# Performance work log

Hardware: AMD Instinct MI355X
Metric: run time of the kernel (lower is better)

## Reference

```python
import jax, jax.numpy as jnp
import numpy as np

T, B, IN = 216, 16384, 8
H1, H2 = 16, 64


def _lstm_scan(xs, h0, c0, Wih, Whh, bih, bhh):
    # xs: [T, B, D_in]; returns all hidden states [T, B, H]
    def step(carry, x_t):
        h, c = carry
        g = x_t @ Wih.T + bih + h @ Whh.T + bhh  # [B, 4H]
        i, f, gg, o = jnp.split(g, 4, axis=-1)
        c = jax.nn.sigmoid(f) * c + jax.nn.sigmoid(i) * jnp.tanh(gg)
        h = jax.nn.sigmoid(o) * jnp.tanh(c)
        return (h, c), h
    (_, _), hs = jax.lax.scan(step, (h0, c0), xs)
    return hs


def setup_inputs() -> dict:
    key = jax.random.key(0)
    ks = jax.random.split(key, 24)
    def rn(k, shape, std):
        return jax.random.normal(k, shape, dtype=jnp.float32) * std
    # PyTorch LSTMCell/Linear default init: U(-1/sqrt(H), 1/sqrt(H)) -> use uniform
    def un(k, shape, bound):
        return jax.random.uniform(k, shape, dtype=jnp.float32, minval=-bound, maxval=bound)
    b1 = 1.0 / np.sqrt(H1)
    b2 = 1.0 / np.sqrt(H2)
    inp = {
        'x': jax.random.normal(ks[0], (T, B, IN), dtype=jnp.float32),
        # initial states: kaiming_normal_ with fan_in = last dim -> std = sqrt(2/fan_in)
        'h0f': rn(ks[1], (B, H1), np.sqrt(2.0 / H1)),
        'c0f': rn(ks[2], (B, H1), np.sqrt(2.0 / H1)),
        'h0b': rn(ks[3], (B, H1), np.sqrt(2.0 / H1)),
        'c0b': rn(ks[4], (B, H1), np.sqrt(2.0 / H1)),
        'h0m': rn(ks[5], (B, H2), np.sqrt(2.0 / H2)),
        'c0m': rn(ks[6], (B, H2), np.sqrt(2.0 / H2)),
        'Wih_f': un(ks[7], (4 * H1, IN), b1), 'Whh_f': un(ks[8], (4 * H1, H1), b1),
        'bih_f': un(ks[9], (4 * H1,), b1), 'bhh_f': un(ks[10], (4 * H1,), b1),
        'Wih_b': un(ks[11], (4 * H1, IN), b1), 'Whh_b': un(ks[12], (4 * H1, H1), b1),
        'bih_b': un(ks[13], (4 * H1,), b1), 'bhh_b': un(ks[14], (4 * H1,), b1),
        'Wih_m': un(ks[15], (4 * H2, 2 * H1), b2), 'Whh_m': un(ks[16], (4 * H2, H2), b2),
        'bih_m': un(ks[17], (4 * H2,), b2), 'bhh_m': un(ks[18], (4 * H2,), b2),
        'Wd': un(ks[19], (1, H2), b2), 'bd': un(ks[20], (1,), b2),
    }
    return inp


def reference(x, h0f, c0f, h0b, c0b, h0m, c0m,
              Wih_f, Whh_f, bih_f, bhh_f,
              Wih_b, Whh_b, bih_b, bhh_b,
              Wih_m, Whh_m, bih_m, bhh_m,
              Wd, bd):
    # forward direction LSTM over time
    hs_f = _lstm_scan(x, h0f, c0f, Wih_f, Whh_f, bih_f, bhh_f)          # [T,B,16]
    # backward direction: run on reversed sequence, then reverse outputs
    hs_b = _lstm_scan(x[::-1], h0b, c0b, Wih_b, Whh_b, bih_b, bhh_b)[::-1]  # [T,B,16]
    mid_in = jnp.concatenate([hs_f, hs_b], axis=-1)                     # [T,B,32]
    hs_m = _lstm_scan(mid_in, h0m, c0m, Wih_m, Whh_m, bih_m, bhh_m)     # [T,B,64]
    # dropout is identity in inference reference; dense 64->1 per step
    out = jnp.einsum('tbh,oh->tbo', hs_m, Wd) + bd                      # [T,B,1]
    return out[:, :, 0].T                                                # [B,T]
```

## Files before the change

### kernel.cpp

```cpp
#include <hip/hip_runtime.h>

#define TT 216
#define BB 16384
#define LOG2E 1.44269504088896340736f

typedef _Float16 h16;
typedef _Float16 half8 __attribute__((ext_vector_type(8)));
typedef _Float16 h4 __attribute__((ext_vector_type(4)));
typedef float f32x4 __attribute__((ext_vector_type(4)));
typedef int i2 __attribute__((ext_vector_type(2)));
typedef int i4 __attribute__((ext_vector_type(4)));

__device__ __forceinline__ float rcp_f(float v) { return __builtin_amdgcn_rcpf(v); }
__device__ __forceinline__ float ex2(float v)   { return __builtin_amdgcn_exp2f(v); }

__device__ __forceinline__ float lstm_up(float pi, float pf, float pg, float po, float& cs)
{
    float ei = ex2(pi), ef = ex2(pf), eg = ex2(pg), eo = ex2(po);
    float Ei = 1.f + ei, Ef = 1.f + ef, Eg = 1.f + eg, Eo = 1.f + eo;
    float EiEg = Ei * Eg;
    float G = fmaf(2.f * LOG2E, Eg, -4.f * LOG2E);
    float N = fmaf(cs, EiEg, Ef * G);
    cs = N * rcp_f(Ef * EiEg);
    float pc = fminf(cs, 60.f);
    float Ec = 1.f + ex2(pc);
    return (Ec - 2.f) * rcp_f(Eo * Ec);
}

__global__ void prep_kernel(
    const float* __restrict__ Wih_f, const float* __restrict__ Whh_f,
    const float* __restrict__ bih_f, const float* __restrict__ bhh_f,
    const float* __restrict__ Wih_b, const float* __restrict__ Whh_b,
    const float* __restrict__ bih_b, const float* __restrict__ bhh_b,
    const float* __restrict__ Wih_m, const float* __restrict__ Whh_m,
    const float* __restrict__ bih_m, const float* __restrict__ bhh_m,
    h16* __restrict__ W1f, h16* __restrict__ W1b, h16* __restrict__ W2)
{
    int gtid = blockIdx.x * blockDim.x + threadIdx.x;
    int gs = gridDim.x * blockDim.x;
    for (int idx = gtid; idx < 64 * 32; idx += gs) {
        int n = idx >> 5, k = idx & 31;
        float a = ((n >> 4) == 2) ? 2.f * LOG2E : -LOG2E;
        float vf = 0.f, vb = 0.f;
        if (k < 8)        { vf = Wih_f[n * 8 + k];       vb = Wih_b[n * 8 + k]; }
        else if (k < 24)  { vf = Whh_f[n * 16 + k - 8];  vb = Whh_b[n * 16 + k - 8]; }
        else if (k == 24) { vf = bih_f[n] + bhh_f[n];    vb = bih_b[n] + bhh_b[n]; }
        W1f[idx] = (h16)(vf * a);
        W1b[idx] = (h16)(vb * a);
    }
    for (int idx = gtid; idx < 256 * 128; idx += gs) {
        int n = idx >> 7, k = idx & 127;
        float a = ((n >> 6) == 2) ? 2.f * LOG2E : -LOG2E;
        float v = 0.f;
        if (k < 32)       v = Wih_m[n * 32 + k];
        else if (k < 96)  v = Whh_m[n * 64 + k - 32];
        else if (k == 96) v = bih_m[n] + bhh_m[n];
        W2[idx] = (h16)(v * a);
    }
}

__global__ __launch_bounds__(256, 2) void small_lstm_kernel(
    const float* __restrict__ x,
    const float* __restrict__ h0f, const float* __restrict__ c0f,
    const float* __restrict__ h0b, const float* __restrict__ c0b,
    const h16* __restrict__ W1f, const h16* __restrict__ W1b,
    h16* __restrict__ hsf, h16* __restrict__ hsb)
{
    const int tid = threadIdx.x;
    const int wv = tid >> 6, lane = tid & 63;
    const int b = lane & 15, q = lane >> 4;

    const int wgid = blockIdx.x * 4 + wv;
    const int dir  = wgid & 1;
    const int base = (wgid >> 1) * 16;

    const float* h0 = dir ? h0b : h0f;
    const float* c0 = dir ? c0b : c0f;
    const h16* W1   = dir ? W1b : W1f;
    h16* hs = dir ? hsb : hsf;

    half8 wf0 = *(const half8*)(W1 + (0 * 16 + b) * 32 + q * 8);
    half8 wf1 = *(const half8*)(W1 + (1 * 16 + b) * 32 + q * 8);
    half8 wf2 = *(const half8*)(W1 + (2 * 16 + b) * 32 + q * 8);
    half8 wf3 = *(const half8*)(W1 + (3 * 16 + b) * 32 + q * 8);

    f32x4 cv = *(const f32x4*)(c0 + (size_t)(base + b) * 16 + q * 4);
    float cs0 = cv[0] * (2.f * LOG2E);
    float cs1 = cv[1] * (2.f * LOG2E);
    float cs2 = cv[2] * (2.f * LOG2E);
    float cs3 = cv[3] * (2.f * LOG2E);

    const int t0 = dir ? (TT - 1) : 0;

    half8 sf;
    if (q == 0) {
        const float* xp = x + ((size_t)t0 * BB + base + b) * 8;
        f32x4 u0 = *(const f32x4*)xp, u1 = *(const f32x4*)(xp + 4);
        sf[0] = (h16)u0[0]; sf[1] = (h16)u0[1]; sf[2] = (h16)u0[2]; sf[3] = (h16)u0[3];
        sf[4] = (h16)u1[0]; sf[5] = (h16)u1[1]; sf[6] = (h16)u1[2]; sf[7] = (h16)u1[3];
    } else if (q == 3) {
        sf[0] = (h16)1.f;
        sf[1] = (h16)0.f; sf[2] = (h16)0.f; sf[3] = (h16)0.f;
        sf[4] = (h16)0.f; sf[5] = (h16)0.f; sf[6] = (h16)0.f; sf[7] = (h16)0.f;
    } else {
        const float* hp = h0 + (size_t)(base + b) * 16 + (q - 1) * 8;
        f32x4 u0 = *(const f32x4*)hp, u1 = *(const f32x4*)(hp + 4);
        sf[0] = (h16)u0[0]; sf[1] = (h16)u0[1]; sf[2] = (h16)u0[2]; sf[3] = (h16)u0[3];
        sf[4] = (h16)u1[0]; sf[5] = (h16)u1[1]; sf[6] = (h16)u1[2]; sf[7] = (h16)u1[3];
    }

    f32x4 xr[4][2];
    if (q == 0) {
#pragma unroll
        for (int u = 1; u <= 3; ++u) {
            int tl = dir ? (TT - 1 - u) : u;
            const float* xp = x + ((size_t)tl * BB + base + b) * 8;
            xr[u][0] = *(const f32x4*)xp;
            xr[u][1] = *(const f32x4*)(xp + 4);
        }
    }

    for (int it = 0; it < TT / 4; ++it) {
#pragma unroll
        for (int j = 0; j < 4; ++j) {
            const int s = it * 4 + j;
            const int t = dir ? (TT - 1 - s) : s;

            f32x4 z0 = {0.f, 0.f, 0.f, 0.f}, z1 = z0, z2 = z0, z3 = z0;
            z0 = __builtin_amdgcn_mfma_f32_16x16x32_f16(wf0, sf, z0, 0, 0, 0);
            z1 = __builtin_amdgcn_mfma_f32_16x16x32_f16(wf1, sf, z1, 0, 0, 0);
            z2 = __builtin_amdgcn_mfma_f32_16x16x32_f16(wf2, sf, z2, 0, 0, 0);
            z3 = __builtin_amdgcn_mfma_f32_16x16x32_f16(wf3, sf, z3, 0, 0, 0);

            half8 xh;
            {
                const f32x4 u0 = xr[(j + 1) & 3][0], u1 = xr[(j + 1) & 3][1];
                xh[0] = (h16)u0[0]; xh[1] = (h16)u0[1]; xh[2] = (h16)u0[2]; xh[3] = (h16)u0[3];
                xh[4] = (h16)u1[0]; xh[5] = (h16)u1[1]; xh[6] = (h16)u1[2]; xh[7] = (h16)u1[3];
            }
            if (q == 0) {
                int ut = (s + 4 < TT) ? (s + 4) : (TT - 1);
                int tl = dir ? (TT - 1 - ut) : ut;
                const float* xp = x + ((size_t)tl * BB + base + b) * 8;
                xr[j][0] = *(const f32x4*)xp;
                xr[j][1] = *(const f32x4*)(xp + 4);
            }

            float hh0 = lstm_up(z0[0], z1[0], z2[0], z3[0], cs0);
            float hh1 = lstm_up(z0[1], z1[1], z2[1], z3[1], cs1);
            float hh2 = lstm_up(z0[2], z1[2], z2[2], z3[2], cs2);
            float hh3 = lstm_up(z0[3], z1[3], z2[3], z3[3], cs3);

            h4 hv;
            hv[0] = (h16)hh0; hv[1] = (h16)hh1; hv[2] = (h16)hh2; hv[3] = (h16)hh3;
            *(h4*)(hs + ((size_t)t * BB + base + b) * 16 + q * 4) = hv;

            i2 pk = __builtin_bit_cast(i2, hv);
            int sp0 = __builtin_amdgcn_ds_swizzle(pk[0], 0x401F);
            int sp1 = __builtin_amdgcn_ds_swizzle(pk[1], 0x401F);

            i4 nw;
            nw[0] = (q == 1) ? sp0 : pk[0];
            nw[1] = (q == 1) ? sp1 : pk[1];
            nw[2] = (q == 1) ? pk[0] : sp0;
            nw[3] = (q == 1) ? pk[1] : sp1;
            half8 nf = __builtin_bit_cast(half8, nw);

            if (q == 0)      sf = xh;
            else if (q != 3) sf = nf;
        }
    }
}

__global__ __launch_bounds__(256, 4) void mid_lstm_kernel(
    const h16* __restrict__ hsf, const h16* __restrict__ hsb,
    const float* __restrict__ h0m, const float* __restrict__ c0m,
    const h16* __restrict__ W2,
    const float* __restrict__ Wd, const float* __restrict__ bdp,
    float* __restrict__ out)
{
    __shared__ __attribute__((aligned(16))) h16 Xs[2][16][104];
    __shared__ float outbuf[16][55];

    const int tid = threadIdx.x;
    const int base = blockIdx.x * 16;
    const int wv = tid >> 6, lane = tid & 63, col = lane & 15, q = lane >> 4;

    half8 bfr[4][3];
    float bp[4];
#pragma unroll
    for (int p = 0; p < 4; ++p) {
        int n = p * 64 + wv * 16 + col;
#pragma unroll
        for (int kt = 0; kt < 3; ++kt)
            bfr[p][kt] = *(const half8*)(W2 + (size_t)n * 128 + kt * 32 + q * 8);
        bp[p] = (float)W2[(size_t)n * 128 + 96];
    }
    half8 dfr[2];
#pragma unroll
    for (int kt = 0; kt < 2; ++kt)
#pragma unroll
        for (int j = 0; j < 8; ++j)
            dfr[kt][j] = (col == 0) ? (h16)Wd[kt * 32 + q * 8 + j] : (h16)0.f;
    const float bdv = bdp[0];

    float cs[4];
#pragma unroll
    for (int r = 0; r < 4; ++r)
        cs[r] = c0m[(size_t)(base + q * 4 + r) * 64 + wv * 16 + col] * (2.f * LOG2E);

    const h16* hsrc = (wv == 1) ? hsb : hsf;
    const int srow = lane >> 1, su8 = (lane & 1) * 8;
    if (wv < 2 && lane < 32) {
        uint4 v = *(const uint4*)(hsrc + ((size_t)0 * BB + base + srow) * 16 + su8);
        *(uint4*)&Xs[0][srow][wv * 16 + su8] = v;
    }
    {
        int row = tid >> 4, u4 = (tid & 15) * 4;
        float4 v = *(const float4*)(h0m + (size_t)(base + row) * 64 + u4);
        h16* d = &Xs[0][row][32 + u4];
        d[0] = (h16)v.x; d[1] = (h16)v.y; d[2] = (h16)v.z; d[3] = (h16)v.w;
    }
    uint4 ra, rb;
    if (wv < 2 && lane < 32) {
        ra = *(const uint4*)(hsrc + ((size_t)1 * BB + base + srow) * 16 + su8);
        rb = *(const uint4*)(hsrc + ((size_t)2 * BB + base + srow) * 16 + su8);
    }
    __syncthreads();

    for (int t = 0; t < TT; ++t) {
        const int cur = t & 1, nxt = cur ^ 1;
        if (wv < 2 && lane < 32) {
            if (t < TT - 1)
                *(uint4*)&Xs[nxt][srow][wv * 16 + su8] = ra;
            ra = rb;
            int tl = (t + 3 < TT) ? (t + 3) : (TT - 1);
            rb = *(const uint4*)(hsrc + ((size_t)tl * BB + base + srow) * 16 + su8);
        }
        half8 af[3];
#pragma unroll
        for (int kt = 0; kt < 3; ++kt)
            af[kt] = *(const half8*)&Xs[cur][col][kt * 32 + q * 8];
        if (wv == 3 && t > 0) {
            f32x4 z = {0.f, 0.f, 0.f, 0.f};
            z = __builtin_amdgcn_mfma_f32_16x16x32_f16(af[1], dfr[0], z, 0, 0, 0);
            z = __builtin_amdgcn_mfma_f32_16x16x32_f16(af[2], dfr[1], z, 0, 0, 0);
            if (col == 0) {
                int tc = (t - 1) % 54;
#pragma unroll
                for (int r = 0; r < 4; ++r)
                    outbuf[q * 4 + r][tc] = z[r] + bdv;
            }
        }
        f32x4 acc[4];
#pragma unroll
        for (int p = 0; p < 4; ++p) {
            f32x4 z = {bp[p], bp[p], bp[p], bp[p]};
            z = __builtin_amdgcn_mfma_f32_16x16x32_f16(af[0], bfr[p][0], z, 0, 0, 0);
            z = __builtin_amdgcn_mfma_f32_16x16x32_f16(af[1], bfr[p][1], z, 0, 0, 0);
            z = __builtin_amdgcn_mfma_f32_16x16x32_f16(af[2], bfr[p][2], z, 0, 0, 0);
            acc[p] = z;
        }
#pragma unroll
        for (int r = 0; r < 4; ++r) {
            float h = lstm_up(acc[0][r], acc[1][r], acc[2][r], acc[3][r], cs[r]);
            Xs[nxt][q * 4 + r][32 + wv * 16 + col] = (h16)h;
        }
        if (t > 0 && (t % 54) == 0) {
            __syncthreads();
            int off = t - 54;
            for (int idx = tid; idx < 16 * 54; idx += 256) {
                int row = idx / 54, cc = idx - row * 54;
                out[(size_t)(base + row) * TT + off + cc] = outbuf[row][cc];
            }
        }
        __syncthreads();
    }
    if (wv == 3) {
        half8 a1 = *(const half8*)&Xs[0][col][32 + q * 8];
        half8 a2 = *(const half8*)&Xs[0][col][64 + q * 8];
        f32x4 z = {0.f, 0.f, 0.f, 0.f};
        z = __builtin_amdgcn_mfma_f32_16x16x32_f16(a1, dfr[0], z, 0, 0, 0);
        z = __builtin_amdgcn_mfma_f32_16x16x32_f16(a2, dfr[1], z, 0, 0, 0);
        if (col == 0)
#pragma unroll
            for (int r = 0; r < 4; ++r)
                outbuf[q * 4 + r][53] = z[r] + bdv;
    }
    __syncthreads();
    for (int idx = tid; idx < 16 * 54; idx += 256) {
        int row = idx / 54, cc = idx - row * 54;
        out[(size_t)(base + row) * TT + 162 + cc] = outbuf[row][cc];
    }
}

extern "C" void kernel_launch(void* const* d_in, const int* in_sizes, int n_in,
                              void* d_out, int out_size, void* d_ws, size_t ws_size,
                              hipStream_t stream)
{
    const float* x     = (const float*)d_in[0];
    const float* h0f   = (const float*)d_in[1];
    const float* c0f   = (const float*)d_in[2];
    const float* h0b   = (const float*)d_in[3];
    const float* c0b   = (const float*)d_in[4];
    const float* h0m   = (const float*)d_in[5];
    const float* c0m   = (const float*)d_in[6];
    const float* Wih_f = (const float*)d_in[7];
    const float* Whh_f = (const float*)d_in[8];
    const float* bih_f = (const float*)d_in[9];
    const float* bhh_f = (const float*)d_in[10];
    const float* Wih_b = (const float*)d_in[11];
    const float* Whh_b = (const float*)d_in[12];
    const float* bih_b = (const float*)d_in[13];
    const float* bhh_b = (const float*)d_in[14];
    const float* Wih_m = (const float*)d_in[15];
    const float* Whh_m = (const float*)d_in[16];
    const float* bih_m = (const float*)d_in[17];
    const float* bhh_m = (const float*)d_in[18];
    const float* Wd    = (const float*)d_in[19];
    const float* bd    = (const float*)d_in[20];

    char* ws = (char*)d_ws;
    h16* W1f = (h16*)(ws + 0);
    h16* W1b = (h16*)(ws + 4096);
    h16* W2  = (h16*)(ws + 8192);
    h16* hsf = (h16*)(ws + 73728);
    h16* hsb = (h16*)(ws + 73728 + (size_t)TT * BB * 16 * 2);

    prep_kernel<<<64, 256, 0, stream>>>(Wih_f, Whh_f, bih_f, bhh_f,
                                        Wih_b, Whh_b, bih_b, bhh_b,
                                        Wih_m, Whh_m, bih_m, bhh_m,
                                        W1f, W1b, W2);
    small_lstm_kernel<<<512, 256, 0, stream>>>(x, h0f, c0f, h0b, c0b,
                                               W1f, W1b, hsf, hsb);
    mid_lstm_kernel<<<1024, 256, 0, stream>>>(hsf, hsb, h0m, c0m, W2,
                                              Wd, bd, (float*)d_out);
}
```

Baseline: 609.1 us.

## Give each wave its own 16-row batch tile in mid LSTM, registers only

```diff
diff --git a/kernel.cpp b/kernel.cpp
--- a/kernel.cpp
+++ b/kernel.cpp
@@ -34,7 +34,8 @@
     const float* __restrict__ bih_b, const float* __restrict__ bhh_b,
     const float* __restrict__ Wih_m, const float* __restrict__ Whh_m,
     const float* __restrict__ bih_m, const float* __restrict__ bhh_m,
-    h16* __restrict__ W1f, h16* __restrict__ W1b, h16* __restrict__ W2)
+    h16* __restrict__ W1f, h16* __restrict__ W1b,
+    h16* __restrict__ W2p, float* __restrict__ bzp)
 {
     int gtid = blockIdx.x * blockDim.x + threadIdx.x;
     int gs = gridDim.x * blockDim.x;
@@ -48,14 +49,23 @@
         W1f[idx] = (h16)(vf * a);
         W1b[idx] = (h16)(vb * a);
     }
-    for (int idx = gtid; idx < 256 * 128; idx += gs) {
-        int n = idx >> 7, k = idx & 127;
-        float a = ((n >> 6) == 2) ? 2.f * LOG2E : -LOG2E;
-        float v = 0.f;
-        if (k < 32)       v = Wih_m[n * 32 + k];
-        else if (k < 96)  v = Whh_m[n * 64 + k - 32];
-        else if (k == 96) v = bih_m[n] + bhh_m[n];
-        W2[idx] = (h16)(v * a);
+    for (int idx = gtid; idx < 256 * 96; idx += gs) {
+        int pm = idx / 96, k = idx - pm * 96;
+        int p = pm >> 4, m = pm & 15;
+        int g = p >> 2, c = p & 3, qq = m >> 2, r = m & 3;
+        int u = ((c >= 2) ? 32 : 0) + (c & 1) * 4 + 8 * qq + r;
+        int n = g * 64 + u;
+        float a = (g == 2) ? 2.f * LOG2E : -LOG2E;
+        float v = (k < 32) ? Wih_m[n * 32 + k] : Whh_m[n * 64 + (k - 32)];
+        W2p[idx] = (h16)(v * a);
+    }
+    for (int pm = gtid; pm < 256; pm += gs) {
+        int p = pm >> 4, m = pm & 15;
+        int g = p >> 2, c = p & 3, qq = m >> 2, r = m & 3;
+        int u = ((c >= 2) ? 32 : 0) + (c & 1) * 4 + 8 * qq + r;
+        int n = g * 64 + u;
+        float a = (g == 2) ? 2.f * LOG2E : -LOG2E;
+        bzp[pm] = (bih_m[n] + bhh_m[n]) * a;
     }
 }
 
@@ -172,125 +182,125 @@
     }
 }
 
-__global__ __launch_bounds__(256, 4) void mid_lstm_kernel(
+__global__ __launch_bounds__(256, 1) void mid_lstm_kernel(
     const h16* __restrict__ hsf, const h16* __restrict__ hsb,
     const float* __restrict__ h0m, const float* __restrict__ c0m,
-    const h16* __restrict__ W2,
+    const h16* __restrict__ W2p, const float* __restrict__ bzp,
     const float* __restrict__ Wd, const float* __restrict__ bdp,
     float* __restrict__ out)
 {
-    __shared__ __attribute__((aligned(16))) h16 Xs[2][16][104];
-    __shared__ float outbuf[16][55];
-
     const int tid = threadIdx.x;
-    const int base = blockIdx.x * 16;
-    const int wv = tid >> 6, lane = tid & 63, col = lane & 15, q = lane >> 4;
-
-    half8 bfr[4][3];
-    float bp[4];
-#pragma unroll
-    for (int p = 0; p < 4; ++p) {
-        int n = p * 64 + wv * 16 + col;
+    const int wv = tid >> 6, lane = tid & 63;
+    const int b = lane & 15, q = lane >> 4;
+
+    const int wgid = blockIdx.x * 4 + wv;
+    const int base = wgid * 16;
+
+    half8 wfr[16][3];
+#pragma unroll
+    for (int p = 0; p < 16; ++p)
 #pragma unroll
         for (int kt = 0; kt < 3; ++kt)
-            bfr[p][kt] = *(const half8*)(W2 + (size_t)n * 128 + kt * 32 + q * 8);
-        bp[p] = (float)W2[(size_t)n * 128 + 96];
-    }
-    half8 dfr[2];
-#pragma unroll
-    for (int kt = 0; kt < 2; ++kt)
-#pragma unroll
-        for (int j = 0; j < 8; ++j)
-            dfr[kt][j] = (col == 0) ? (h16)Wd[kt * 32 + q * 8 + j] : (h16)0.f;
+            wfr[p][kt] = *(const half8*)(W2p + (size_t)(p * 16 + b) * 96 + kt * 32 + q * 8);
+    f32x4 bz[16];
+#pragma unroll
+    for (int p = 0; p < 16; ++p)
+        bz[p] = *(const f32x4*)(bzp + p * 16 + q * 4);
+    half8 df1, df2;
+#pragma unroll
+    for (int j = 0; j < 8; ++j) {
+        df1[j] = (b == 0) ? (h16)Wd[q * 8 + j] : (h16)0.f;
+        df2[j] = (b == 0) ? (h16)Wd[32 + q * 8 + j] : (h16)0.f;
+    }
     const float bdv = bdp[0];
 
-    float cs[4];
-#pragma unroll
-    for (int r = 0; r < 4; ++r)
-        cs[r] = c0m[(size_t)(base + q * 4 + r) * 64 + wv * 16 + col] * (2.f * LOG2E);
-
-    const h16* hsrc = (wv == 1) ? hsb : hsf;
-    const int srow = lane >> 1, su8 = (lane & 1) * 8;
-    if (wv < 2 && lane < 32) {
-        uint4 v = *(const uint4*)(hsrc + ((size_t)0 * BB + base + srow) * 16 + su8);
-        *(uint4*)&Xs[0][srow][wv * 16 + su8] = v;
-    }
+    f32x4 cs[4];
+#pragma unroll
+    for (int c = 0; c < 4; ++c) {
+        int off = ((c >= 2) ? 32 : 0) + (c & 1) * 4 + 8 * q;
+        f32x4 v = *(const f32x4*)(c0m + (size_t)(base + b) * 64 + off);
+        cs[c][0] = v[0] * (2.f * LOG2E); cs[c][1] = v[1] * (2.f * LOG2E);
+        cs[c][2] = v[2] * (2.f * LOG2E); cs[c][3] = v[3] * (2.f * LOG2E);
+    }
+
+    half8 nf1, nf2;
     {
-        int row = tid >> 4, u4 = (tid & 15) * 4;
-        float4 v = *(const float4*)(h0m + (size_t)(base + row) * 64 + u4);
-        h16* d = &Xs[0][row][32 + u4];
-        d[0] = (h16)v.x; d[1] = (h16)v.y; d[2] = (h16)v.z; d[3] = (h16)v.w;
-    }
-    uint4 ra, rb;
-    if (wv < 2 && lane < 32) {
-        ra = *(const uint4*)(hsrc + ((size_t)1 * BB + base + srow) * 16 + su8);
-        rb = *(const uint4*)(hsrc + ((size_t)2 * BB + base + srow) * 16 + su8);
-    }
-    __syncthreads();
-
-    for (int t = 0; t < TT; ++t) {
-        const int cur = t & 1, nxt = cur ^ 1;
-        if (wv < 2 && lane < 32) {
-            if (t < TT - 1)
-                *(uint4*)&Xs[nxt][srow][wv * 16 + su8] = ra;
-            ra = rb;
-            int tl = (t + 3 < TT) ? (t + 3) : (TT - 1);
-            rb = *(const uint4*)(hsrc + ((size_t)tl * BB + base + srow) * 16 + su8);
+        const float* hp = h0m + (size_t)(base + b) * 64 + q * 8;
+        f32x4 a0 = *(const f32x4*)hp, a1 = *(const f32x4*)(hp + 4);
+        f32x4 a2 = *(const f32x4*)(hp + 32), a3 = *(const f32x4*)(hp + 36);
+        nf1[0] = (h16)a0[0]; nf1[1] = (h16)a0[1]; nf1[2] = (h16)a0[2]; nf1[3] = (h16)a0[3];
+        nf1[4] = (h16)a1[0]; nf1[5] = (h16)a1[1]; nf1[6] = (h16)a1[2]; nf1[7] = (h16)a1[3];
+        nf2[0] = (h16)a2[0]; nf2[1] = (h16)a2[1]; nf2[2] = (h16)a2[2]; nf2[3] = (h16)a2[3];
+        nf2[4] = (h16)a3[0]; nf2[5] = (h16)a3[1]; nf2[6] = (h16)a3[2]; nf2[7] = (h16)a3[3];
+    }
+
+    const h16* hsq = (q < 2) ? hsf : hsb;
+    const size_t hoff = (size_t)(base + b) * 16 + (q & 1) * 8;
+    uint4 hx[4];
+#pragma unroll
+    for (int u = 0; u < 4; ++u)
+        hx[u] = *(const uint4*)(hsq + (size_t)u * BB * 16 + hoff);
+
+    f32x4 ot;
+    for (int it = 0; it < TT / 4; ++it) {
+#pragma unroll
+        for (int j = 0; j < 4; ++j) {
+            const int s = it * 4 + j;
+            const half8 sf0 = __builtin_bit_cast(half8, hx[j]);
+
+            h4 pkc[4];
+#pragma unroll
+            for (int c = 0; c < 4; ++c) {
+                f32x4 z0 = bz[0 * 4 + c], z1 = bz[1 * 4 + c];
+                f32x4 z2 = bz[2 * 4 + c], z3 = bz[3 * 4 + c];
+                z0 = __builtin_amdgcn_mfma_f32_16x16x32_f16(wfr[0 * 4 + c][0], sf0, z0, 0, 0, 0);
+                z0 = __builtin_amdgcn_mfma_f32_16x16x32_f16(wfr[0 * 4 + c][1], nf1, z0, 0, 0, 0);
+                z0 = __builtin_amdgcn_mfma_f32_16x16x32_f16(wfr[0 * 4 + c][2], nf2, z0, 0, 0, 0);
+                z1 = __builtin_amdgcn_mfma_f32_16x16x32_f16(wfr[1 * 4 + c][0], sf0, z1, 0, 0, 0);
+                z1 = __builtin_amdgcn_mfma_f32_16x16x32_f16(wfr[1 * 4 + c][1], nf1, z1, 0, 0, 0);
+                z1 = __builtin_amdgcn_mfma_f32_16x16x32_f16(wfr[1 * 4 + c][2], nf2, z1, 0, 0, 0);
+                z2 = __builtin_amdgcn_mfma_f32_16x16x32_f16(wfr[2 * 4 + c][0], sf0, z2, 0, 0, 0);
+                z2 = __builtin_amdgcn_mfma_f32_16x16x32_f16(wfr[2 * 4 + c][1], nf1, z2, 0, 0, 0);
+                z2 = __builtin_amdgcn_mfma_f32_16x16x32_f16(wfr[2 * 4 + c][2], nf2, z2, 0, 0, 0);
+                z3 = __builtin_amdgcn_mfma_f32_16x16x32_f16(wfr[3 * 4 + c][0], sf0, z3, 0, 0, 0);
+                z3 = __builtin_amdgcn_mfma_f32_16x16x32_f16(wfr[3 * 4 + c][1], nf1, z3, 0, 0, 0);
+                z3 = __builtin_amdgcn_mfma_f32_16x16x32_f16(wfr[3 * 4 + c][2], nf2, z3, 0, 0, 0);
+
+                float c0v = cs[c][0];
+                float hh0 = lstm_up(z0[0], z1[0], z2[0], z3[0], c0v); cs[c][0] = c0v;
+                float c1v = cs[c][1];
+                float hh1 = lstm_up(z0[1], z1[1], z2[1], z3[1], c1v); cs[c][1] = c1v;
+                float c2v = cs[c][2];
+                float hh2 = lstm_up(z0[2], z1[2], z2[2], z3[2], c2v); cs[c][2] = c2v;
+                float c3v = cs[c][3];
+                float hh3 = lstm_up(z0[3], z1[3], z2[3], z3[3], c3v); cs[c][3] = c3v;
+
+                h4 pk;
+                pk[0] = (h16)hh0; pk[1] = (h16)hh1; pk[2] = (h16)hh2; pk[3] = (h16)hh3;
+                pkc[c] = pk;
+            }
+            {
+                i2 p0 = __builtin_bit_cast(i2, pkc[0]), p1 = __builtin_bit_cast(i2, pkc[1]);
+                i2 p2 = __builtin_bit_cast(i2, pkc[2]), p3 = __builtin_bit_cast(i2, pkc[3]);
+                i4 n1, n2;
+                n1[0] = p0[0]; n1[1] = p0[1]; n1[2] = p1[0]; n1[3] = p1[1];
+                n2[0] = p2[0]; n2[1] = p2[1]; n2[2] = p3[0]; n2[3] = p3[1];
+                nf1 = __builtin_bit_cast(half8, n1);
+                nf2 = __builtin_bit_cast(half8, n2);
+            }
+            {
+                int sl = (s + 4 < TT) ? (s + 4) : (TT - 1);
+                hx[j] = *(const uint4*)(hsq + (size_t)sl * BB * 16 + hoff);
+            }
+            {
+                f32x4 zd = {0.f, 0.f, 0.f, 0.f};
+                zd = __builtin_amdgcn_mfma_f32_16x16x32_f16(df1, nf1, zd, 0, 0, 0);
+                zd = __builtin_amdgcn_mfma_f32_16x16x32_f16(df2, nf2, zd, 0, 0, 0);
+                ot[j] = zd[0] + bdv;
+            }
         }
-        half8 af[3];
-#pragma unroll
-        for (int kt = 0; kt < 3; ++kt)
-            af[kt] = *(const half8*)&Xs[cur][col][kt * 32 + q * 8];
-        if (wv == 3 && t > 0) {
-            f32x4 z = {0.f, 0.f, 0.f, 0.f};
-            z = __builtin_amdgcn_mfma_f32_16x16x32_f16(af[1], dfr[0], z, 0, 0, 0);
-            z = __builtin_amdgcn_mfma_f32_16x16x32_f16(af[2], dfr[1], z, 0, 0, 0);
-            if (col == 0) {
-                int tc = (t - 1) % 54;
-#pragma unroll
-                for (int r = 0; r < 4; ++r)
-                    outbuf[q * 4 + r][tc] = z[r] + bdv;
-            }
-        }
-        f32x4 acc[4];
-#pragma unroll
-        for (int p = 0; p < 4; ++p) {
-            f32x4 z = {bp[p], bp[p], bp[p], bp[p]};
-            z = __builtin_amdgcn_mfma_f32_16x16x32_f16(af[0], bfr[p][0], z, 0, 0, 0);
-            z = __builtin_amdgcn_mfma_f32_16x16x32_f16(af[1], bfr[p][1], z, 0, 0, 0);
-            z = __builtin_amdgcn_mfma_f32_16x16x32_f16(af[2], bfr[p][2], z, 0, 0, 0);
-            acc[p] = z;
-        }
-#pragma unroll
-        for (int r = 0; r < 4; ++r) {
-            float h = lstm_up(acc[0][r], acc[1][r], acc[2][r], acc[3][r], cs[r]);
-            Xs[nxt][q * 4 + r][32 + wv * 16 + col] = (h16)h;
-        }
-        if (t > 0 && (t % 54) == 0) {
-            __syncthreads();
-            int off = t - 54;
-            for (int idx = tid; idx < 16 * 54; idx += 256) {
-                int row = idx / 54, cc = idx - row * 54;
-                out[(size_t)(base + row) * TT + off + cc] = outbuf[row][cc];
-            }
-        }
-        __syncthreads();
-    }
-    if (wv == 3) {
-        half8 a1 = *(const half8*)&Xs[0][col][32 + q * 8];
-        half8 a2 = *(const half8*)&Xs[0][col][64 + q * 8];
-        f32x4 z = {0.f, 0.f, 0.f, 0.f};
-        z = __builtin_amdgcn_mfma_f32_16x16x32_f16(a1, dfr[0], z, 0, 0, 0);
-        z = __builtin_amdgcn_mfma_f32_16x16x32_f16(a2, dfr[1], z, 0, 0, 0);
-        if (col == 0)
-#pragma unroll
-            for (int r = 0; r < 4; ++r)
-                outbuf[q * 4 + r][53] = z[r] + bdv;
-    }
-    __syncthreads();
-    for (int idx = tid; idx < 16 * 54; idx += 256) {
-        int row = idx / 54, cc = idx - row * 54;
-        out[(size_t)(base + row) * TT + 162 + cc] = outbuf[row][cc];
+        if (q == 0)
+            *(f32x4*)(out + (size_t)(base + b) * TT + it * 4) = ot;
     }
 }
 
@@ -321,18 +331,19 @@
     const float* bd    = (const float*)d_in[20];
 
     char* ws = (char*)d_ws;
-    h16* W1f = (h16*)(ws + 0);
-    h16* W1b = (h16*)(ws + 4096);
-    h16* W2  = (h16*)(ws + 8192);
-    h16* hsf = (h16*)(ws + 73728);
-    h16* hsb = (h16*)(ws + 73728 + (size_t)TT * BB * 16 * 2);
+    h16*   W1f = (h16*)(ws + 0);
+    h16*   W1b = (h16*)(ws + 4096);
+    h16*   W2p = (h16*)(ws + 8192);
+    float* bzp = (float*)(ws + 57344);
+    h16*   hsf = (h16*)(ws + 65536);
+    h16*   hsb = (h16*)(ws + 65536 + (size_t)TT * BB * 16 * 2);
 
     prep_kernel<<<64, 256, 0, stream>>>(Wih_f, Whh_f, bih_f, bhh_f,
                                         Wih_b, Whh_b, bih_b, bhh_b,
                                         Wih_m, Whh_m, bih_m, bhh_m,
-                                        W1f, W1b, W2);
+                                        W1f, W1b, W2p, bzp);
     small_lstm_kernel<<<512, 256, 0, stream>>>(x, h0f, c0f, h0b, c0b,
                                                W1f, W1b, hsf, hsb);
-    mid_lstm_kernel<<<1024, 256, 0, stream>>>(hsf, hsb, h0m, c0m, W2,
-                                              Wd, bd, (float*)d_out);
-}
+    mid_lstm_kernel<<<256, 256, 0, stream>>>(hsf, hsb, h0m, c0m, W2p, bzp,
+                                             Wd, bd, (float*)d_out);
+}
```

Measured after the change: 873.1 us. 43.3% more time.
